# Optimization experiments

Hardware: AMD Instinct MI355X
Metric: run time of the kernel (lower is better)

Reference implementation:

```python
import jax, jax.numpy as jnp
import numpy as np

B, T, H, L = 64, 512, 512, 4


def setup_inputs() -> dict:
    key = jax.random.key(0)
    k0, k1, k2 = jax.random.split(key, 3)
    s = 1.0 / np.sqrt(H)
    x = jax.random.normal(k0, (B, T, H), dtype=jnp.float32)
    # kernel [in, 4H] and recurrent kernel [H, 4H] per layer; gate order i,f,c,o (Keras)
    W = jax.random.uniform(k1, (L, H, 4 * H), jnp.float32, -s, s)
    U = jax.random.uniform(k2, (L, H, 4 * H), jnp.float32, -s, s)
    # unit_forget_bias=True: forget-gate bias initialized to ones
    b = jnp.tile(jnp.concatenate([jnp.zeros(H), jnp.ones(H), jnp.zeros(2 * H)]).astype(jnp.float32), (L, 1))
    return {"x": x, "W": W, "U": U, "b": b}


def _lstm_layer(x_tbd, W, U, b):
    """x_tbd: [T,B,D]. Returns (h_seq [T,B,H], h_final [B,H])."""
    Bx = x_tbd.shape[1]
    Hd = U.shape[0]
    xW = x_tbd @ W + b  # precompute input projection: [T,B,4H]

    def step(carry, zx):
        h, c = carry
        z = zx + h @ U
        i, f, g, o = jnp.split(z, 4, axis=-1)
        c = jax.nn.sigmoid(f) * c + jax.nn.sigmoid(i) * jnp.tanh(g)
        h = jax.nn.sigmoid(o) * jnp.tanh(c)
        return (h, c), h

    h0 = jnp.zeros((Bx, Hd), x_tbd.dtype)
    (h_fin, _), h_seq = jax.lax.scan(step, (h0, h0), xW)
    return h_seq, h_fin


def reference(x, W, U, b):
    # training=False => dropout disabled. Layers 1..L-1 have residual wrappers.
    inp = jnp.swapaxes(x, 0, 1)  # [T,B,D]
    first_h = None
    nl = W.shape[0]
    for l in range(nl):
        h_seq, h_fin = _lstm_layer(inp, W[l], U[l], b[l])
        inp = h_seq + inp if l >= 1 else h_seq  # residual wrapper on layers >=1
        if l == 0:
            first_h = h_fin
    rnn_output = jnp.swapaxes(inp, 0, 1)  # [B,T,H]
    # original returns output[1] (first cell's final h) replicated num_layers times
    states = jnp.broadcast_to(first_h, (nl,) + first_h.shape)
    return (rnn_output, states)
```

## Files before the change

kernel.cpp:

```cpp
#include <hip/hip_runtime.h>
#include <stddef.h>


typedef float          f32x4 __attribute__((ext_vector_type(4)));
typedef short          s16x8 __attribute__((ext_vector_type(8)));
typedef unsigned short u16;
typedef u16            u16x4 __attribute__((ext_vector_type(4)));
typedef _Float16       f16x4 __attribute__((ext_vector_type(4)));
typedef unsigned long long u64;
typedef u64            u64x2 __attribute__((ext_vector_type(2)));

__device__ __forceinline__ u16 f2bf(float f) {
    unsigned int u = __builtin_bit_cast(unsigned int, f);
    u += 0x7FFFu + ((u >> 16) & 1u);
    return (u16)(u >> 16);
}
__device__ __forceinline__ float sig(float x) { return 1.f / (1.f + __expf(-x)); }
__device__ __forceinline__ float th(float x)  { return 2.f / (1.f + __expf(-2.f * x)) - 1.f; }
__device__ __forceinline__ u64 pk2(float a, float b) {
    return (u64)__builtin_bit_cast(unsigned, a) | ((u64)__builtin_bit_cast(unsigned, b) << 32);
}
__device__ __forceinline__ float lo32(u64 v) { return __builtin_bit_cast(float, (unsigned)v); }
__device__ __forceinline__ float hi32(u64 v) { return __builtin_bit_cast(float, (unsigned)(v >> 32)); }
__device__ __forceinline__ u64 ald(const u64* p) {
    return __hip_atomic_load(p, __ATOMIC_RELAXED, __HIP_MEMORY_SCOPE_AGENT);
}
__device__ __forceinline__ void ast(u64* p, u64 v) {
    __hip_atomic_store(p, v, __ATOMIC_RELAXED, __HIP_MEMORY_SCOPE_AGENT);
}

__device__ __forceinline__ void pollflags(const int* p, bool active) {
    while (1) {
        int v = 1;
        if (active) v = __hip_atomic_load(p, __ATOMIC_RELAXED, __HIP_MEMORY_SCOPE_AGENT);
        if (__ballot(v != 0) == ~0ull) break;
    }
}

#define NFLG 6299648
__global__ void init_flags(int* __restrict__ flg) {
    int i = blockIdx.x * 256 + threadIdx.x;
    if (i < NFLG) flg[i] = 0;
}

__global__ void convert_x(const float* __restrict__ x, u64* __restrict__ XB) {
#pragma unroll
    for (int i = 0; i < 8; ++i) {
        int f = blockIdx.x * 2048 + i * 256 + threadIdx.x;
        int h4 = f & 127, b = (f >> 7) & 63, t = f >> 13;
        int wg = h4 >> 2, q = h4 & 3;
        f32x4 v = *(const f32x4*)(x + ((size_t)b * 512 + t) * 512 + h4 * 4);
        u16x4 o = { f2bf(v[0]), f2bf(v[1]), f2bf(v[2]), f2bf(v[3]) };
        XB[(size_t)t * 8192 + wg * 256 + b * 4 + q] = __builtin_bit_cast(u64, o);
    }
}

__global__ void convert_wu(const float* __restrict__ W, const float* __restrict__ U,
                           u16* __restrict__ WBF, u16* __restrict__ UBF) {
    __shared__ float tl[32][33];
    const int l = blockIdx.z & 3, which = blockIdx.z >> 2;
    const float* src = (which ? U : W) + (size_t)l * 512 * 2048;
    u16* dst = (which ? UBF : WBF) + (size_t)l * 2048 * 512;
    const int n0 = blockIdx.x * 32, k0 = blockIdx.y * 32;
    const int tid = threadIdx.x;
    const int r = tid >> 3, c4 = (tid & 7) * 4;
    f32x4 v = *(const f32x4*)(src + (size_t)(k0 + r) * 2048 + n0 + c4);
    tl[r][c4 + 0] = v[0]; tl[r][c4 + 1] = v[1]; tl[r][c4 + 2] = v[2]; tl[r][c4 + 3] = v[3];
    __syncthreads();
    u16x4 o = { f2bf(tl[c4 + 0][r]), f2bf(tl[c4 + 1][r]), f2bf(tl[c4 + 2][r]), f2bf(tl[c4 + 3][r]) };
    *(u16x4*)(dst + (size_t)(n0 + r) * 512 + k0 + c4) = o;
}

__global__ __launch_bounds__(256, 1) void fused(const u64* __restrict__ XB,
                                                const u16* __restrict__ WBF,
                                                const u16* __restrict__ UBF,
                                                const float* __restrict__ bias,
                                                float* __restrict__ INP,
                                                int* __restrict__ flgh,
                                                int* __restrict__ flgx,
                                                int* __restrict__ flgp,
                                                u64* __restrict__ hring,
                                                u64* __restrict__ XWR,
                                                u64* __restrict__ INPB,
                                                float* __restrict__ states) {
    extern __shared__ char lds[];
    char* wlds = lds;

    const int tid = threadIdx.x, lane = tid & 63, wave = tid >> 6;
    const int m_l = lane & 15, q16 = lane >> 4;
    const int swz = (m_l & 7) << 4;
    const int qh = q16 >> 1, ql = (q16 & 1) << 1;
    const bool rec = blockIdx.x < 128;
    const int l  = rec ? (blockIdx.x & 3) : ((blockIdx.x - 128) & 3);
    const int wg = rec ? (blockIdx.x >> 2) : ((blockIdx.x - 128) >> 2);
    const int brow = wave * 16 + m_l;
    const int u0 = wg * 16 + q16 * 4;

    {
        const u16* wsrc = (rec ? UBF : WBF) + (size_t)l * 1048576;
#pragma unroll
        for (int i = 0; i < 16; ++i) {
            int idx = tid + i * 256;
            int row = idx >> 6, seg = idx & 63;
            int g = row >> 4, up = row & 15;
            s16x8 v = *(const s16x8*)(wsrc + ((size_t)(g * 512 + wg * 16 + up)) * 512 + seg * 8);
            *(s16x8*)(wlds + row * 1024 + ((seg * 16) ^ ((row & 7) << 4))) = v;
        }
    }
    __syncthreads();

    if (rec) {
        u64 xr[4];
        pollflags(flgp + (((size_t)(l * 512 + 0) * 32 + wg) << 5), true);
        {
            const u64* p = XWR + ((size_t)(l * 8 + 0) * 32 + wg) * 1024 + tid * 4;
#pragma unroll
            for (int k = 0; k < 4; ++k) xr[k] = ald(p + k);
        }
        float cr[4] = {0.f, 0.f, 0.f, 0.f};
        float hprev[4] = {0.f, 0.f, 0.f, 0.f};

        for (int t = 0; t <= 512; ++t) {
            u64 rrv0 = 0, rrv1 = 0;
            u64* ip = (u64*)INP + (size_t)(t > 0 ? t - 1 : 0) * 16384 +
                      (size_t)brow * 256 + (u0 >> 1);
            if (t > 0 && l > 0) { rrv0 = ald(ip); rrv1 = ald(ip + 1); }

            if (t > 0) pollflags(flgh + (((size_t)(l * 513 + t - 1) * 32 + (lane & 31)) << 5), lane < 32);

            f32x4 acc[4] = {};
            if (t > 0 && t < 512) {
                const u64* hs = hring + (((size_t)((t - 1) & 1) * 4 + l) << 13);
                u64 hlo[16], hhi[16];
#pragma unroll
                for (int kf = 0; kf < 16; ++kf) {
                    const u64* fp = hs + ((kf * 2 + qh) << 8) + brow * 4 + ql;
                    hlo[kf] = ald(fp); hhi[kf] = ald(fp + 1);
                }
#pragma unroll
                for (int kf = 0; kf < 16; ++kf) {
                    u64x2 hv = { hlo[kf], hhi[kf] };
                    s16x8 hf = __builtin_bit_cast(s16x8, hv);
                    const int col = (kf * 64 + q16 * 16) ^ swz;
#pragma unroll
                    for (int g = 0; g < 4; ++g) {
                        s16x8 wf = *(const s16x8*)(wlds + (g * 16 + m_l) * 1024 + col);
                        acc[g] = __builtin_amdgcn_mfma_f32_16x16x32_bf16(wf, hf, acc[g], 0, 0, 0);
                    }
                }
            }

            float hn[4] = {0.f, 0.f, 0.f, 0.f};
            if (t < 512) {
#pragma unroll
                for (int r = 0; r < 4; ++r) {
                    f16x4 xw = __builtin_bit_cast(f16x4, xr[r]);
                    float zi = acc[0][r] + (float)xw[0];
                    float zf = acc[1][r] + (float)xw[1];
                    float zg = acc[2][r] + (float)xw[2];
                    float zo = acc[3][r] + (float)xw[3];
                    float cc = sig(zf) * cr[r] + sig(zi) * th(zg);
                    cr[r] = cc;
                    hn[r] = sig(zo) * th(cc);
                }
                u16x4 hb = { f2bf(hn[0]), f2bf(hn[1]), f2bf(hn[2]), f2bf(hn[3]) };
                ast(hring + (((size_t)(t & 1) * 4 + l) << 13) + wg * 256 + brow * 4 + q16,
                    __builtin_bit_cast(u64, hb));
                asm volatile("s_waitcnt vmcnt(0)" ::: "memory");
                __syncthreads();
                if (tid == 0)
                    __hip_atomic_store(flgh + (((size_t)(l * 513 + t) * 32 + wg) << 5), 1,
                                       __ATOMIC_RELAXED, __HIP_MEMORY_SCOPE_AGENT);
            }

            if (t > 0) {
                if (l < 3 && t >= 17)
                    pollflags(flgp + (((size_t)((l + 1) * 512 + t - 17) * 32 + (lane & 31)) << 5), lane < 32);
                float o[4];
#pragma unroll
                for (int r = 0; r < 4; ++r) o[r] = hprev[r];
                if (l > 0) {
                    o[0] += lo32(rrv0); o[1] += hi32(rrv0);
                    o[2] += lo32(rrv1); o[3] += hi32(rrv1);
                }
                ast(ip,     pk2(o[0], o[1]));
                ast(ip + 1, pk2(o[2], o[3]));
                if (l < 3) {
                    u16x4 ob = { f2bf(o[0]), f2bf(o[1]), f2bf(o[2]), f2bf(o[3]) };
                    ast(INPB + (((size_t)l * 16 + ((t - 1) & 15)) << 13) + wg * 256 + brow * 4 + q16,
                        __builtin_bit_cast(u64, ob));
                }
                if (l == 0 && t == 512) {
                    f32x4 sv = { o[0], o[1], o[2], o[3] };
#pragma unroll
                    for (int rep = 0; rep < 4; ++rep)
                        *(f32x4*)&states[(size_t)rep * 32768 + (size_t)brow * 512 + u0] = sv;
                }
                asm volatile("s_waitcnt vmcnt(0)" ::: "memory");
                __syncthreads();
                if (tid == 0 && l < 3)
                    __hip_atomic_store(flgx + (((size_t)(l * 513 + t) * 32 + wg) << 5), 1,
                                       __ATOMIC_RELAXED, __HIP_MEMORY_SCOPE_AGENT);
            }

            if (t < 511) {
                pollflags(flgp + (((size_t)(l * 512 + t + 1) * 32 + wg) << 5), true);
                const u64* p = XWR + ((size_t)(l * 8 + ((t + 1) & 7)) * 32 + wg) * 1024 + tid * 4;
#pragma unroll
                for (int k = 0; k < 4; ++k) xr[k] = ald(p + k);
            }
#pragma unroll
            for (int r = 0; r < 4; ++r) if (t < 512) hprev[r] = hn[r];
        }
    } else {
        float bj[4][4];
#pragma unroll
        for (int g = 0; g < 4; ++g)
#pragma unroll
            for (int r = 0; r < 4; ++r)
                bj[g][r] = bias[(size_t)l * 2048 + g * 512 + u0 + r];

        for (int t = 0; t < 512; ++t) {
            if (l > 0) pollflags(flgx + (((size_t)((l - 1) * 513 + t + 1) * 32 + (lane & 31)) << 5), lane < 32);
            u64 xlo[16], xhi[16];
            if (l == 0) {
                const u64* xs = XB + (size_t)t * 8192;
#pragma unroll
                for (int kf = 0; kf < 16; ++kf) {
                    const u64* fp = xs + ((kf * 2 + qh) << 8) + brow * 4 + ql;
                    xlo[kf] = fp[0]; xhi[kf] = fp[1];
                }
            } else {
                const u64* xs = INPB + (((size_t)(l - 1) * 16 + (t & 15)) << 13);
#pragma unroll
                for (int kf = 0; kf < 16; ++kf) {
                    const u64* fp = xs + ((kf * 2 + qh) << 8) + brow * 4 + ql;
                    xlo[kf] = ald(fp); xhi[kf] = ald(fp + 1);
                }
            }
            if (t >= 8) pollflags(flgh + (((size_t)(l * 513 + t - 8) * 32 + wg) << 5), true);

            f32x4 acc[4] = {};
#pragma unroll
            for (int kf = 0; kf < 16; ++kf) {
                u64x2 xv = { xlo[kf], xhi[kf] };
                s16x8 xf = __builtin_bit_cast(s16x8, xv);
                const int col = (kf * 64 + q16 * 16) ^ swz;
#pragma unroll
                for (int g = 0; g < 4; ++g) {
                    s16x8 wf = *(const s16x8*)(wlds + (g * 16 + m_l) * 1024 + col);
                    acc[g] = __builtin_amdgcn_mfma_f32_16x16x32_bf16(wf, xf, acc[g], 0, 0, 0);
                }
            }

            u64* xd = XWR + ((size_t)(l * 8 + (t & 7)) * 32 + wg) * 1024 + tid * 4;
#pragma unroll
            for (int r = 0; r < 4; ++r) {
                f16x4 pk = { (_Float16)(acc[0][r] + bj[0][r]), (_Float16)(acc[1][r] + bj[1][r]),
                             (_Float16)(acc[2][r] + bj[2][r]), (_Float16)(acc[3][r] + bj[3][r]) };
                ast(xd + r, __builtin_bit_cast(u64, pk));
            }
            asm volatile("s_waitcnt vmcnt(0)" ::: "memory");
            __syncthreads();
            if (tid == 0)
                __hip_atomic_store(flgp + (((size_t)(l * 512 + t) * 32 + wg) << 5), 1,
                                   __ATOMIC_RELAXED, __HIP_MEMORY_SCOPE_AGENT);
        }
    }
}

__global__ void transpose_out(const float* __restrict__ inp, float* __restrict__ out) {
#pragma unroll
    for (int i = 0; i < 8; ++i) {
        int f = blockIdx.x * 2048 + i * 256 + threadIdx.x;
        int h4 = f & 127, t = (f >> 7) & 511, b = f >> 16;
        f32x4 v = *(const f32x4*)(inp + ((size_t)t * 64 + b) * 512 + h4 * 4);
        *(f32x4*)(out + ((size_t)b * 512 + t) * 512 + h4 * 4) = v;
    }
}

extern "C" void kernel_launch(void* const* d_in, const int* in_sizes, int n_in,
                              void* d_out, int out_size, void* d_ws, size_t ws_size,
                              hipStream_t stream) {
    const float* x = (const float*)d_in[0];
    const float* W = (const float*)d_in[1];
    const float* U = (const float*)d_in[2];
    const float* b = (const float*)d_in[3];
    float* out = (float*)d_out;
    char* ws = (char*)d_ws;

    constexpr size_t XB_OFF   = 0;
    constexpr size_t INP_OFF  = 33554432;
    constexpr size_t WBF_OFF  = INP_OFF + 67108864;
    constexpr size_t UBF_OFF  = WBF_OFF + 8388608;
    constexpr size_t FLGH_OFF = UBF_OFF + 8388608;
    constexpr size_t FLGX_OFF = FLGH_OFF + 8404992;
    constexpr size_t FLGP_OFF = FLGX_OFF + 8404992;
    constexpr size_t HR_OFF   = FLGP_OFF + 8388608;
    constexpr size_t XWR_OFF  = HR_OFF + 524288;
    constexpr size_t INPB_OFF = XWR_OFF + 8388608;

    u64*      XB  = (u64*)(ws + XB_OFF);
    float*    INP = (float*)(ws + INP_OFF);
    u16*      WBF = (u16*)(ws + WBF_OFF);
    u16*      UBF = (u16*)(ws + UBF_OFF);
    int*      flgh = (int*)(ws + FLGH_OFF);
    int*      flgx = (int*)(ws + FLGX_OFF);
    int*      flgp = (int*)(ws + FLGP_OFF);
    u64*      hring = (u64*)(ws + HR_OFF);
    u64*      XWR  = (u64*)(ws + XWR_OFF);
    u64*      INPB = (u64*)(ws + INPB_OFF);

    constexpr int FUSED_LDS = 65536;
    static int attr_done = 0;
    if (!attr_done) {
        (void)hipFuncSetAttribute((const void*)fused,
                                  hipFuncAttributeMaxDynamicSharedMemorySize, FUSED_LDS);
        attr_done = 1;
    }

    init_flags<<<(NFLG + 255) / 256, 256, 0, stream>>>(flgh);
    convert_x<<<2048, 256, 0, stream>>>(x, XB);
    convert_wu<<<dim3(64, 16, 8), 256, 0, stream>>>(W, U, WBF, UBF);
    fused<<<256, 256, FUSED_LDS, stream>>>(XB, WBF, UBF, b, INP, flgh, flgx, flgp,
                                           hring, XWR, INPB, out + 16777216);
    transpose_out<<<2048, 256, 0, stream>>>(INP, out);
}
```

Baseline: 2.963 ms.

## Merge flag polls and defer flag releases to cut per-step barriers in LSTM pipeline

The recurrent blocks now wait on their three dependency flags (previous h step, downstream projection consumer, next xW tile) in one combined polling loop split across lanes, instead of three separate polls. The next xW prefetch is moved ahead of the MFMA work. Flag releases are delayed by one step and folded into the barrier that already exists: the projection block raises step t-1 at step t, and the recurrent block raises its residual-output flag together with the h flag. This removes one vmcnt wait plus __syncthreads per step in each role, at the cost of a one-step delay in dependency signalling and more complex end-of-loop handling.

```diff
diff --git a/kernel.cpp b/kernel.cpp
--- a/kernel.cpp
+++ b/kernel.cpp
@@ -27,6 +27,9 @@
 }
 __device__ __forceinline__ void ast(u64* p, u64 v) {
     __hip_atomic_store(p, v, __ATOMIC_RELAXED, __HIP_MEMORY_SCOPE_AGENT);
+}
+__device__ __forceinline__ void raiseflag(int* p) {
+    __hip_atomic_store(p, 1, __ATOMIC_RELAXED, __HIP_MEMORY_SCOPE_AGENT);
 }
 
 __device__ __forceinline__ void pollflags(const int* p, bool active) {
@@ -126,7 +129,35 @@
                       (size_t)brow * 256 + (u0 >> 1);
             if (t > 0 && l > 0) { rrv0 = ald(ip); rrv1 = ald(ip + 1); }
 
-            if (t > 0) pollflags(flgh + (((size_t)(l * 513 + t - 1) * 32 + (lane & 31)) << 5), lane < 32);
+            {
+                const int tb = (t >= 17) ? t - 17 : 0;
+                const int tc = (t < 511) ? t + 1 : 0;
+                const int* pA;
+                bool actA;
+                if (lane < 32) {
+                    pA = flgh + (((size_t)(l * 513 + (t > 0 ? t - 1 : 0)) * 32 + lane) << 5);
+                    actA = (t > 0);
+                } else {
+                    const int lp = (l < 3) ? l + 1 : 3;
+                    pA = flgp + (((size_t)(lp * 512 + tb) * 32 + (lane - 32)) << 5);
+                    actA = (l < 3) && (t >= 17);
+                }
+                const int* pB = flgp + (((size_t)(l * 512 + tc) * 32 + wg) << 5);
+                const bool actB = (lane == 63) && (t < 511);
+                while (1) {
+                    int v = 1;
+                    if (actA) v = __hip_atomic_load(pA, __ATOMIC_RELAXED, __HIP_MEMORY_SCOPE_AGENT);
+                    if (actB) v &= __hip_atomic_load(pB, __ATOMIC_RELAXED, __HIP_MEMORY_SCOPE_AGENT);
+                    if (__ballot(v != 0) == ~0ull) break;
+                }
+            }
+
+            u64 xrn[4] = {0, 0, 0, 0};
+            if (t < 511) {
+                const u64* p = XWR + ((size_t)(l * 8 + ((t + 1) & 7)) * 32 + wg) * 1024 + tid * 4;
+#pragma unroll
+                for (int k = 0; k < 4; ++k) xrn[k] = ald(p + k);
+            }
 
             f32x4 acc[4] = {};
             if (t > 0 && t < 512) {
@@ -168,14 +199,19 @@
                     __builtin_bit_cast(u64, hb));
                 asm volatile("s_waitcnt vmcnt(0)" ::: "memory");
                 __syncthreads();
-                if (tid == 0)
-                    __hip_atomic_store(flgh + (((size_t)(l * 513 + t) * 32 + wg) << 5), 1,
-                                       __ATOMIC_RELAXED, __HIP_MEMORY_SCOPE_AGENT);
+                if (tid == 0) {
+                    raiseflag(flgh + (((size_t)(l * 513 + t) * 32 + wg) << 5));
+                    if (l < 3 && t >= 2)
+                        raiseflag(flgx + (((size_t)(l * 513 + t - 1) * 32 + wg) << 5));
+                }
+            } else {
+                asm volatile("s_waitcnt vmcnt(0)" ::: "memory");
+                __syncthreads();
+                if (tid == 0 && l < 3)
+                    raiseflag(flgx + (((size_t)(l * 513 + 511) * 32 + wg) << 5));
             }
 
             if (t > 0) {
-                if (l < 3 && t >= 17)
-                    pollflags(flgp + (((size_t)((l + 1) * 512 + t - 17) * 32 + (lane & 31)) << 5), lane < 32);
                 float o[4];
 #pragma unroll
                 for (int r = 0; r < 4; ++r) o[r] = hprev[r];
@@ -196,21 +232,19 @@
                     for (int rep = 0; rep < 4; ++rep)
                         *(f32x4*)&states[(size_t)rep * 32768 + (size_t)brow * 512 + u0] = sv;
                 }
-                asm volatile("s_waitcnt vmcnt(0)" ::: "memory");
-                __syncthreads();
-                if (tid == 0 && l < 3)
-                    __hip_atomic_store(flgx + (((size_t)(l * 513 + t) * 32 + wg) << 5), 1,
-                                       __ATOMIC_RELAXED, __HIP_MEMORY_SCOPE_AGENT);
-            }
-
+                if (t == 512) {
+                    asm volatile("s_waitcnt vmcnt(0)" ::: "memory");
+                    __syncthreads();
+                    if (tid == 0 && l < 3)
+                        raiseflag(flgx + (((size_t)(l * 513 + 512) * 32 + wg) << 5));
+                }
+            }
+#pragma unroll
+            for (int r = 0; r < 4; ++r) if (t < 512) hprev[r] = hn[r];
             if (t < 511) {
-                pollflags(flgp + (((size_t)(l * 512 + t + 1) * 32 + wg) << 5), true);
-                const u64* p = XWR + ((size_t)(l * 8 + ((t + 1) & 7)) * 32 + wg) * 1024 + tid * 4;
-#pragma unroll
-                for (int k = 0; k < 4; ++k) xr[k] = ald(p + k);
-            }
-#pragma unroll
-            for (int r = 0; r < 4; ++r) if (t < 512) hprev[r] = hn[r];
+#pragma unroll
+                for (int k = 0; k < 4; ++k) xr[k] = xrn[k];
+            }
         }
     } else {
         float bj[4][4];
@@ -221,7 +255,23 @@
                 bj[g][r] = bias[(size_t)l * 2048 + g * 512 + u0 + r];
 
         for (int t = 0; t < 512; ++t) {
-            if (l > 0) pollflags(flgx + (((size_t)((l - 1) * 513 + t + 1) * 32 + (lane & 31)) << 5), lane < 32);
+            {
+                const int* pA;
+                bool actA;
+                if (lane < 32) {
+                    pA = flgx + (((size_t)((l > 0 ? l - 1 : 0) * 513 + t + 1) * 32 + lane) << 5);
+                    actA = (l > 0);
+                } else {
+                    pA = flgh + (((size_t)(l * 513 + (t >= 8 ? t - 8 : 0)) * 32 + wg) << 5);
+                    actA = (lane == 32) && (t >= 8);
+                }
+                while (1) {
+                    int v = 1;
+                    if (actA) v = __hip_atomic_load(pA, __ATOMIC_RELAXED, __HIP_MEMORY_SCOPE_AGENT);
+                    if (__ballot(v != 0) == ~0ull) break;
+                }
+            }
+
             u64 xlo[16], xhi[16];
             if (l == 0) {
                 const u64* xs = XB + (size_t)t * 8192;
@@ -238,7 +288,6 @@
                     xlo[kf] = ald(fp); xhi[kf] = ald(fp + 1);
                 }
             }
-            if (t >= 8) pollflags(flgh + (((size_t)(l * 513 + t - 8) * 32 + wg) << 5), true);
 
             f32x4 acc[4] = {};
 #pragma unroll
@@ -253,6 +302,11 @@
                 }
             }
 
+            asm volatile("s_waitcnt vmcnt(0)" ::: "memory");
+            __syncthreads();
+            if (tid == 0 && t > 0)
+                raiseflag(flgp + (((size_t)(l * 512 + t - 1) * 32 + wg) << 5));
+
             u64* xd = XWR + ((size_t)(l * 8 + (t & 7)) * 32 + wg) * 1024 + tid * 4;
 #pragma unroll
             for (int r = 0; r < 4; ++r) {
@@ -260,12 +314,11 @@
                              (_Float16)(acc[2][r] + bj[2][r]), (_Float16)(acc[3][r] + bj[3][r]) };
                 ast(xd + r, __builtin_bit_cast(u64, pk));
             }
-            asm volatile("s_waitcnt vmcnt(0)" ::: "memory");
-            __syncthreads();
-            if (tid == 0)
-                __hip_atomic_store(flgp + (((size_t)(l * 512 + t) * 32 + wg) << 5), 1,
-                                   __ATOMIC_RELAXED, __HIP_MEMORY_SCOPE_AGENT);
         }
+        asm volatile("s_waitcnt vmcnt(0)" ::: "memory");
+        __syncthreads();
+        if (tid == 0)
+            raiseflag(flgp + (((size_t)(l * 512 + 511) * 32 + wg) << 5));
     }
 }
 
```

New measurement: 2.736 ms. 7.6% less time.
